# Kernel tuning notes

Measured on AMD Instinct MI355X. Metric: run time of the kernel, lower is better.

The kernel has to match this reference:

```python
import jax, jax.numpy as jnp
import numpy as np
from jax import lax

DN = ('NCHW', 'OIHW', 'NCHW')

def _conv(x, w, pad):
    return lax.conv_general_dilated(x, w, (1, 1), [(pad, pad), (pad, pad)], dimension_numbers=DN)

def setup_inputs() -> dict:
    key = jax.random.key(0)
    ks = jax.random.split(key, 4)
    B, H, W = 8, 512, 512
    K = 3  # k_size
    image = jax.random.normal(ks[0], (B, 1, H, W), dtype=jnp.float32)
    refer = jax.random.normal(ks[1], (B, 1, H, W), dtype=jnp.float32)
    # filter-generating network params (Conv 5x5: 2->32, LeakyReLU(0.1), Conv 5x5: 32->9)
    w1 = jax.random.normal(ks[2], (32, 2, 5, 5), dtype=jnp.float32) * 0.05
    b1 = jnp.zeros((32,), dtype=jnp.float32)
    w2 = jax.random.normal(ks[3], (K * K, 32, 5, 5), dtype=jnp.float32) * 0.05
    b2 = jnp.zeros((K * K,), dtype=jnp.float32)
    return {'image': image, 'refer': refer, 'w1': w1, 'b1': b1, 'w2': w2, 'b2': b2}

def reference(image, refer, w1, b1, w2, b2):
    K = 3
    x = jnp.concatenate([image, refer], axis=1)                      # [B,2,H,W]
    h = _conv(x, w1, 2) + b1[None, :, None, None]                    # [B,32,H,W]
    h = jnp.where(h >= 0, h, 0.1 * h)                                # LeakyReLU(0.1)
    filters = _conv(h, w2, 2) + b2[None, :, None, None]              # [B,K*K,H,W]
    # im2col via identity conv: weight eye(K*K) reshaped to [K*K,1,K,K]
    eye_w = jnp.eye(K * K, dtype=image.dtype).reshape(K * K, 1, K, K)
    expanded = _conv(image, eye_w, 1)                                # [B,K*K,H,W]
    out = jnp.sum(expanded * filters, axis=1, keepdims=True)         # [B,1,H,W]
    return out
```

## Files before the change

kernel.cpp:

```cpp
#include <hip/hip_runtime.h>
#include <hip/hip_bf16.h>


typedef __attribute__((ext_vector_type(8))) short bf16x8;
typedef __attribute__((ext_vector_type(4))) float f32x4;

#define HH 512
#define WW 512
#define TILE 16
#define XS_H 24
#define XS_W 24
#define HS_R 20
#define HS_C 20
#define PXS 40
#define UBYTES (400 * PXS * 2)

__device__ __forceinline__ unsigned short f2bf(float x) {
    union { float f; unsigned int u; } v; v.f = x;
    unsigned int u = v.u;
    u += 0x7FFFu + ((u >> 16) & 1u);
    return (unsigned short)(u >> 16);
}

__device__ __forceinline__ unsigned int pack_bf2(float a, float b) {
    __hip_bfloat162 h2 = __float22bfloat162_rn(make_float2(a, b));
    union { __hip_bfloat162 h; unsigned int u; } cv; cv.h = h2;
    return cv.u;
}

__global__ void dynfilt_prep(const float* __restrict__ w1,
                             const float* __restrict__ w2,
                             unsigned short* __restrict__ w1c,
                             unsigned short* __restrict__ w2t)
{
    int gid = blockIdx.x * 256 + threadIdx.x;
    for (int i = gid; i < 32 * 64; i += 8192) {
        int ch = i >> 6, k = i & 63;
        int tap = k >> 1, ci = k & 1;
        w1c[i] = (k < 50) ? f2bf(w1[(ch * 2 + ci) * 25 + tap]) : (unsigned short)0;
    }
    for (int i = gid; i < 28 * 16 * 32; i += 8192) {
        int p = i & 31;
        int f = (i >> 5) & 15;
        int tap = i >> 9;
        int ch = (p & 1) * 16 + (p >> 1);
        unsigned short v = 0;
        if (tap < 25 && f < 9) v = f2bf(w2[(f * 32 + ch) * 25 + tap]);
        w2t[i] = v;
    }
}

__global__
__attribute__((amdgpu_flat_work_group_size(256, 256), amdgpu_waves_per_eu(4)))
void dynfilt_main(const float* __restrict__ image,
                  const float* __restrict__ refer,
                  const float* __restrict__ b1,
                  const float* __restrict__ b2,
                  const unsigned short* __restrict__ w1c,
                  const unsigned short* __restrict__ w2t,
                  float* __restrict__ out)
{
    __shared__ float xs0[XS_H][XS_W];
    __shared__ unsigned int pxc[XS_H * XS_W];
    __shared__ __align__(16) unsigned char ubuf[UBYTES];
    unsigned short* xcol = (unsigned short*)ubuf;
    unsigned short* hs   = (unsigned short*)ubuf;

    const int t   = threadIdx.x;
    const int gx0 = blockIdx.x * TILE;
    const int gy0 = blockIdx.y * TILE;
    const int b   = blockIdx.z;

    #pragma unroll 1
    for (int idx = t; idx < XS_H * XS_W; idx += 256) {
        int r = idx / XS_W, c = idx - (idx / XS_W) * XS_W;
        int gy = gy0 - 4 + r, gx = gx0 - 4 + c;
        float vi = 0.f, vr = 0.f;
        if ((unsigned)gy < HH && (unsigned)gx < WW) {
            size_t o = ((size_t)b * HH + gy) * WW + gx;
            vi = image[o];
            vr = refer[o];
        }
        xs0[r][c] = vi;
        pxc[idx]  = pack_bf2(vi, vr);
    }

    const int lane = t & 63;
    const int wv   = t >> 6;
    const int n    = lane & 15;
    const int kg   = lane >> 4;

    bf16x8 bfr[2][2];
    #pragma unroll
    for (int nt = 0; nt < 2; ++nt)
        #pragma unroll
        for (int s = 0; s < 2; ++s)
            bfr[nt][s] = *(const bf16x8*)(w1c + (nt * 16 + n) * 64 + s * 32 + kg * 8);

    f32x4 d[7][2];
    #pragma unroll
    for (int m = 0; m < 7; ++m) {
        d[m][0] = (f32x4){0.f, 0.f, 0.f, 0.f};
        d[m][1] = (f32x4){0.f, 0.f, 0.f, 0.f};
    }

    __syncthreads();
    #pragma unroll 1
    for (int it = 0; it < 2; ++it) {
        int px = it * 256 + t;
        if (px < HS_R * HS_C) {
            int r = px / HS_C, c = px - (px / HS_C) * HS_C;
            const unsigned int* pb = pxc + r * XS_W + c;
            unsigned int pk[16];
            #pragma unroll
            for (int tap = 0; tap < 16; ++tap) {
                int dy = tap / 5, dx = tap - dy * 5;
                pk[tap] = pb[dy * XS_W + dx];
            }
            unsigned int* dst = (unsigned int*)(xcol + px * PXS);
            #pragma unroll
            for (int w8 = 0; w8 < 4; ++w8)
                ((uint4*)dst)[w8] = make_uint4(pk[4 * w8], pk[4 * w8 + 1],
                                               pk[4 * w8 + 2], pk[4 * w8 + 3]);
        }
    }
    __syncthreads();

    #pragma unroll
    for (int m = 0; m < 7; ++m) {
        int mt = m * 4 + wv;
        if (mt < 25) {
            bf16x8 a0 = *(const bf16x8*)(xcol + (mt * 16 + n) * PXS + kg * 8);
            d[m][0] = __builtin_amdgcn_mfma_f32_16x16x32_bf16(a0, bfr[0][0], d[m][0], 0, 0, 0);
            d[m][1] = __builtin_amdgcn_mfma_f32_16x16x32_bf16(a0, bfr[1][0], d[m][1], 0, 0, 0);
        }
    }
    __syncthreads();

    #pragma unroll 1
    for (int it = 0; it < 2; ++it) {
        int px = it * 256 + t;
        if (px < HS_R * HS_C) {
            int r = px / HS_C, c = px - (px / HS_C) * HS_C;
            const unsigned int* pb = pxc + r * XS_W + c;
            unsigned int pk[16];
            #pragma unroll
            for (int tp = 0; tp < 9; ++tp) {
                int tap = 16 + tp;
                int dy = tap / 5, dx = tap - dy * 5;
                pk[tp] = pb[dy * XS_W + dx];
            }
            #pragma unroll
            for (int tp = 9; tp < 16; ++tp) pk[tp] = 0;
            unsigned int* dst = (unsigned int*)(xcol + px * PXS);
            #pragma unroll
            for (int w8 = 0; w8 < 4; ++w8)
                ((uint4*)dst)[w8] = make_uint4(pk[4 * w8], pk[4 * w8 + 1],
                                               pk[4 * w8 + 2], pk[4 * w8 + 3]);
        }
    }
    __syncthreads();

    #pragma unroll
    for (int m = 0; m < 7; ++m) {
        int mt = m * 4 + wv;
        if (mt < 25) {
            bf16x8 a1 = *(const bf16x8*)(xcol + (mt * 16 + n) * PXS + kg * 8);
            d[m][0] = __builtin_amdgcn_mfma_f32_16x16x32_bf16(a1, bfr[0][1], d[m][0], 0, 0, 0);
            d[m][1] = __builtin_amdgcn_mfma_f32_16x16x32_bf16(a1, bfr[1][1], d[m][1], 0, 0, 0);
        }
    }
    __syncthreads();

    {
        float bb0 = b1[n], bb1 = b1[16 + n];
        #pragma unroll
        for (int m = 0; m < 7; ++m) {
            int mt = m * 4 + wv;
            if (mt < 25) {
                #pragma unroll
                for (int r = 0; r < 4; ++r) {
                    int px = mt * 16 + kg * 4 + r;
                    int pr = px / HS_C, pc = px - pr * HS_C;
                    int gy = gy0 - 2 + pr, gx = gx0 - 2 + pc;
                    bool inb = ((unsigned)gy < HH) & ((unsigned)gx < WW);
                    float h0 = d[m][0][r] + bb0;
                    float h1 = d[m][1][r] + bb1;
                    h0 = (h0 >= 0.f) ? h0 : 0.1f * h0;
                    h1 = (h1 >= 0.f) ? h1 : 0.1f * h1;
                    if (!inb) { h0 = 0.f; h1 = 0.f; }
                    *(unsigned int*)(hs + px * PXS + 2 * n) = pack_bf2(h0, h1);
                }
            }
        }
    }
    __syncthreads();

    int bofs[7];
    #pragma unroll
    for (int q = 0; q < 7; ++q) {
        int tap = 4 * q + kg;
        if (tap > 24) tap = 0;
        int dy = tap / 5, dx = tap - dy * 5;
        bofs[q] = (dy * HS_C + dx) * (PXS * 2);
    }
    const char* bb[4];
    #pragma unroll
    for (int i = 0; i < 4; ++i)
        bb[i] = (const char*)hs + ((wv * 4 + i) * HS_C + n) * (PXS * 2);

    f32x4 acc[4];
    #pragma unroll
    for (int i = 0; i < 4; ++i) acc[i] = (f32x4){0.f, 0.f, 0.f, 0.f};

    #pragma unroll
    for (int q = 0; q < 7; ++q) {
        bf16x8 afr[4];
        #pragma unroll
        for (int g = 0; g < 4; ++g)
            afr[g] = *(const bf16x8*)(w2t + ((4 * q + kg) * 16 + n) * 32 + g * 8);
        #pragma unroll
        for (int i = 0; i < 4; ++i) {
            const char* ba = bb[i] + bofs[q];
            #pragma unroll
            for (int g = 0; g < 4; ++g) {
                bf16x8 bfrag = *(const bf16x8*)(ba + g * 16);
                acc[i] = __builtin_amdgcn_mfma_f32_16x16x32_bf16(afr[g], bfrag, acc[i], 0, 0, 0);
            }
        }
    }

    float b2r[4];
    int fyr[4], fxr[4];
    #pragma unroll
    for (int r2 = 0; r2 < 4; ++r2) {
        int f = kg * 4 + r2;
        b2r[r2] = (f < 9) ? b2[f] : 0.f;
        int fy = f / 3;
        fyr[r2] = fy; fxr[r2] = f - fy * 3;
    }
    #pragma unroll
    for (int i = 0; i < 4; ++i) {
        int py = wv * 4 + i;
        float partial = 0.f;
        #pragma unroll
        for (int r2 = 0; r2 < 4; ++r2) {
            float img = xs0[py + fyr[r2] + 3][n + fxr[r2] + 3];
            partial += (acc[i][r2] + b2r[r2]) * img;
        }
        partial += __shfl_down(partial, 16, 64);
        partial += __shfl_down(partial, 32, 64);
        if (lane < 16)
            out[((size_t)b * HH + gy0 + py) * WW + gx0 + n] = partial;
    }
}

extern "C" void kernel_launch(void* const* d_in, const int* in_sizes, int n_in,
                              void* d_out, int out_size, void* d_ws, size_t ws_size,
                              hipStream_t stream) {
    const float* image = (const float*)d_in[0];
    const float* refer = (const float*)d_in[1];
    const float* w1    = (const float*)d_in[2];
    const float* b1    = (const float*)d_in[3];
    const float* w2    = (const float*)d_in[4];
    const float* b2    = (const float*)d_in[5];

    unsigned short* w1c = (unsigned short*)d_ws;
    unsigned short* w2t = (unsigned short*)((char*)d_ws + 4096);

    hipLaunchKernelGGL(dynfilt_prep, dim3(32), dim3(256), 0, stream, w1, w2, w1c, w2t);

    dim3 grid(WW / TILE, HH / TILE, 8);
    hipLaunchKernelGGL(dynfilt_main, grid, dim3(256), 0, stream,
                       image, refer, b1, b2, w1c, w2t, (float*)d_out);
}
```

Baseline: 169.5 us.

## Gather conv1 A-fragments directly from LDS and remap conv2 K-dimension over channels

Conv1 no longer materialises an im2col buffer in shared memory in two passes with four barriers. Each lane now gathers its four packed pixel dwords straight from the packed-input tile using precomputed tap offsets, and issues both K-halves of the MFMA in one loop. Conv2 is reorganised so each MFMA's K dimension spans the 32 channels of a single tap, iterating over 25 taps instead of 7 groups of 4 taps each with 4 sub-MFMAs. This removes the padded-tap MFMAs and the redundant weight rows, and the prep kernel shrinks to match. The cost is scattered 4-byte LDS reads in place of vector loads, plus a dedicated hs buffer that no longer aliases.

```diff
diff --git a/kernel.cpp b/kernel.cpp
--- a/kernel.cpp
+++ b/kernel.cpp
@@ -13,7 +13,6 @@
 #define HS_R 20
 #define HS_C 20
 #define PXS 40
-#define UBYTES (400 * PXS * 2)
 
 __device__ __forceinline__ unsigned short f2bf(float x) {
     union { float f; unsigned int u; } v; v.f = x;
@@ -26,6 +25,13 @@
     __hip_bfloat162 h2 = __float22bfloat162_rn(make_float2(a, b));
     union { __hip_bfloat162 h; unsigned int u; } cv; cv.h = h2;
     return cv.u;
+}
+
+__device__ __forceinline__ bf16x8 dw4_to_frag(unsigned int d0, unsigned int d1,
+                                              unsigned int d2, unsigned int d3) {
+    union { unsigned int u[4]; bf16x8 f; } cv;
+    cv.u[0] = d0; cv.u[1] = d1; cv.u[2] = d2; cv.u[3] = d3;
+    return cv.f;
 }
 
 __global__ void dynfilt_prep(const float* __restrict__ w1,
@@ -39,14 +45,12 @@
         int tap = k >> 1, ci = k & 1;
         w1c[i] = (k < 50) ? f2bf(w1[(ch * 2 + ci) * 25 + tap]) : (unsigned short)0;
     }
-    for (int i = gid; i < 28 * 16 * 32; i += 8192) {
+    for (int i = gid; i < 25 * 16 * 32; i += 8192) {
         int p = i & 31;
         int f = (i >> 5) & 15;
         int tap = i >> 9;
         int ch = (p & 1) * 16 + (p >> 1);
-        unsigned short v = 0;
-        if (tap < 25 && f < 9) v = f2bf(w2[(f * 32 + ch) * 25 + tap]);
-        w2t[i] = v;
+        w2t[i] = (f < 9) ? f2bf(w2[(f * 32 + ch) * 25 + tap]) : (unsigned short)0;
     }
 }
 
@@ -62,9 +66,7 @@
 {
     __shared__ float xs0[XS_H][XS_W];
     __shared__ unsigned int pxc[XS_H * XS_W];
-    __shared__ __align__(16) unsigned char ubuf[UBYTES];
-    unsigned short* xcol = (unsigned short*)ubuf;
-    unsigned short* hs   = (unsigned short*)ubuf;
+    __shared__ __align__(16) unsigned short hs[HS_R * HS_C * PXS];
 
     const int t   = threadIdx.x;
     const int gx0 = blockIdx.x * TILE;
@@ -84,6 +86,7 @@
         xs0[r][c] = vi;
         pxc[idx]  = pack_bf2(vi, vr);
     }
+    __syncthreads();
 
     const int lane = t & 63;
     const int wv   = t >> 6;
@@ -97,6 +100,22 @@
         for (int s = 0; s < 2; ++s)
             bfr[nt][s] = *(const bf16x8*)(w1c + (nt * 16 + n) * 64 + s * 32 + kg * 8);
 
+    int t0o[4], t1o[4];
+    unsigned int t1m[4];
+    #pragma unroll
+    for (int j = 0; j < 4; ++j) {
+        int tap0 = kg * 4 + j;
+        t0o[j] = (tap0 / 5) * XS_W + tap0 % 5;
+        int tap1 = 16 + kg * 4 + j;
+        int vld  = (tap1 <= 24) ? 1 : 0;
+        int tc   = vld ? tap1 : 0;
+        t1o[j] = (tc / 5) * XS_W + tc % 5;
+        t1m[j] = vld ? 0xFFFFFFFFu : 0u;
+    }
+
+    int px0 = wv * 16 + n;
+    int pr = px0 / 20, pc = px0 - (px0 / 20) * 20;
+
     f32x4 d[7][2];
     #pragma unroll
     for (int m = 0; m < 7; ++m) {
@@ -104,73 +123,27 @@
         d[m][1] = (f32x4){0.f, 0.f, 0.f, 0.f};
     }
 
-    __syncthreads();
-    #pragma unroll 1
-    for (int it = 0; it < 2; ++it) {
-        int px = it * 256 + t;
-        if (px < HS_R * HS_C) {
-            int r = px / HS_C, c = px - (px / HS_C) * HS_C;
-            const unsigned int* pb = pxc + r * XS_W + c;
-            unsigned int pk[16];
-            #pragma unroll
-            for (int tap = 0; tap < 16; ++tap) {
-                int dy = tap / 5, dx = tap - dy * 5;
-                pk[tap] = pb[dy * XS_W + dx];
-            }
-            unsigned int* dst = (unsigned int*)(xcol + px * PXS);
-            #pragma unroll
-            for (int w8 = 0; w8 < 4; ++w8)
-                ((uint4*)dst)[w8] = make_uint4(pk[4 * w8], pk[4 * w8 + 1],
-                                               pk[4 * w8 + 2], pk[4 * w8 + 3]);
-        }
-    }
-    __syncthreads();
-
     #pragma unroll
     for (int m = 0; m < 7; ++m) {
         int mt = m * 4 + wv;
         if (mt < 25) {
-            bf16x8 a0 = *(const bf16x8*)(xcol + (mt * 16 + n) * PXS + kg * 8);
+            const unsigned int* base = pxc + (pr * XS_W + pc);
+            unsigned int a0d[4], a1d[4];
+            #pragma unroll
+            for (int j = 0; j < 4; ++j) a0d[j] = base[t0o[j]];
+            #pragma unroll
+            for (int j = 0; j < 4; ++j) a1d[j] = base[t1o[j]] & t1m[j];
+            bf16x8 a0 = dw4_to_frag(a0d[0], a0d[1], a0d[2], a0d[3]);
+            bf16x8 a1 = dw4_to_frag(a1d[0], a1d[1], a1d[2], a1d[3]);
             d[m][0] = __builtin_amdgcn_mfma_f32_16x16x32_bf16(a0, bfr[0][0], d[m][0], 0, 0, 0);
+            d[m][0] = __builtin_amdgcn_mfma_f32_16x16x32_bf16(a1, bfr[0][1], d[m][0], 0, 0, 0);
             d[m][1] = __builtin_amdgcn_mfma_f32_16x16x32_bf16(a0, bfr[1][0], d[m][1], 0, 0, 0);
-        }
-    }
-    __syncthreads();
-
-    #pragma unroll 1
-    for (int it = 0; it < 2; ++it) {
-        int px = it * 256 + t;
-        if (px < HS_R * HS_C) {
-            int r = px / HS_C, c = px - (px / HS_C) * HS_C;
-            const unsigned int* pb = pxc + r * XS_W + c;
-            unsigned int pk[16];
-            #pragma unroll
-            for (int tp = 0; tp < 9; ++tp) {
-                int tap = 16 + tp;
-                int dy = tap / 5, dx = tap - dy * 5;
-                pk[tp] = pb[dy * XS_W + dx];
-            }
-            #pragma unroll
-            for (int tp = 9; tp < 16; ++tp) pk[tp] = 0;
-            unsigned int* dst = (unsigned int*)(xcol + px * PXS);
-            #pragma unroll
-            for (int w8 = 0; w8 < 4; ++w8)
-                ((uint4*)dst)[w8] = make_uint4(pk[4 * w8], pk[4 * w8 + 1],
-                                               pk[4 * w8 + 2], pk[4 * w8 + 3]);
-        }
-    }
-    __syncthreads();
-
-    #pragma unroll
-    for (int m = 0; m < 7; ++m) {
-        int mt = m * 4 + wv;
-        if (mt < 25) {
-            bf16x8 a1 = *(const bf16x8*)(xcol + (mt * 16 + n) * PXS + kg * 8);
-            d[m][0] = __builtin_amdgcn_mfma_f32_16x16x32_bf16(a1, bfr[0][1], d[m][0], 0, 0, 0);
             d[m][1] = __builtin_amdgcn_mfma_f32_16x16x32_bf16(a1, bfr[1][1], d[m][1], 0, 0, 0);
         }
-    }
-    __syncthreads();
+        pc += 4; pr += 3;
+        int w = (pc >= 20) ? 1 : 0;
+        pc -= 20 * w; pr += w;
+    }
 
     {
         float bb0 = b1[n], bb1 = b1[16 + n];
@@ -181,8 +154,8 @@
                 #pragma unroll
                 for (int r = 0; r < 4; ++r) {
                     int px = mt * 16 + kg * 4 + r;
-                    int pr = px / HS_C, pc = px - pr * HS_C;
-                    int gy = gy0 - 2 + pr, gx = gx0 - 2 + pc;
+                    int prr = px / HS_C, pcc = px - prr * HS_C;
+                    int gy = gy0 - 2 + prr, gx = gx0 - 2 + pcc;
                     bool inb = ((unsigned)gy < HH) & ((unsigned)gx < WW);
                     float h0 = d[m][0][r] + bb0;
                     float h1 = d[m][1][r] + bb1;
@@ -196,37 +169,23 @@
     }
     __syncthreads();
 
-    int bofs[7];
-    #pragma unroll
-    for (int q = 0; q < 7; ++q) {
-        int tap = 4 * q + kg;
-        if (tap > 24) tap = 0;
-        int dy = tap / 5, dx = tap - dy * 5;
-        bofs[q] = (dy * HS_C + dx) * (PXS * 2);
-    }
-    const char* bb[4];
+    const char* bbrow[4];
     #pragma unroll
     for (int i = 0; i < 4; ++i)
-        bb[i] = (const char*)hs + ((wv * 4 + i) * HS_C + n) * (PXS * 2);
+        bbrow[i] = (const char*)hs + (((wv * 4 + i) * HS_C + n) * PXS + kg * 8) * 2;
 
     f32x4 acc[4];
     #pragma unroll
     for (int i = 0; i < 4; ++i) acc[i] = (f32x4){0.f, 0.f, 0.f, 0.f};
 
     #pragma unroll
-    for (int q = 0; q < 7; ++q) {
-        bf16x8 afr[4];
-        #pragma unroll
-        for (int g = 0; g < 4; ++g)
-            afr[g] = *(const bf16x8*)(w2t + ((4 * q + kg) * 16 + n) * 32 + g * 8);
+    for (int tap = 0; tap < 25; ++tap) {
+        bf16x8 afr = *(const bf16x8*)(w2t + (tap * 16 + n) * 32 + kg * 8);
+        const int sofs = ((tap / 5) * HS_C + tap % 5) * (PXS * 2);
         #pragma unroll
         for (int i = 0; i < 4; ++i) {
-            const char* ba = bb[i] + bofs[q];
-            #pragma unroll
-            for (int g = 0; g < 4; ++g) {
-                bf16x8 bfrag = *(const bf16x8*)(ba + g * 16);
-                acc[i] = __builtin_amdgcn_mfma_f32_16x16x32_bf16(afr[g], bfrag, acc[i], 0, 0, 0);
-            }
+            bf16x8 bfrag = *(const bf16x8*)(bbrow[i] + sofs);
+            acc[i] = __builtin_amdgcn_mfma_f32_16x16x32_bf16(afr, bfrag, acc[i], 0, 0, 0);
         }
     }
 
```

Result: faster. 158.1 us (-6.7%).
